# Optimization experiments

Hardware: AMD Instinct MI355X
Metric: run time of the kernel (lower is better)

## Reference

```python
import jax, jax.numpy as jnp
import numpy as np

X_SIZE, Y_SIZE, C_SIZE, H = 4, 2, 3, 128
B, C_CTX, T = 4, 512, 512


def _xavier(key, shape):
    fan_in, fan_out = shape[0], shape[1]
    a = jnp.sqrt(6.0 / (fan_in + fan_out))
    return jax.random.uniform(key, shape, jnp.float32, -a, a)


def setup_inputs() -> dict:
    key = jax.random.key(0)
    ks = jax.random.split(key, 9)
    return {
        "context_x": jax.random.normal(ks[0], (B, C_CTX, X_SIZE), jnp.float32),
        "context_y": jax.random.normal(ks[1], (B, C_CTX, Y_SIZE), jnp.float32),
        "target_x": jax.random.normal(ks[2], (B, T, X_SIZE), jnp.float32),
        "W_in": _xavier(ks[3], (C_SIZE + Y_SIZE, H)),
        "b_in": jnp.zeros((H,), jnp.float32),
        "W_ctx": _xavier(ks[4], (C_SIZE, H)),
        "b_ctx": jnp.zeros((H,), jnp.float32),
        "W_tgt": _xavier(ks[5], (H, H)),
        "b_tgt": jnp.zeros((H,), jnp.float32),
    }


def reference(context_x, context_y, target_x, W_in, b_in, W_ctx, b_ctx, W_tgt, b_tgt):
    ctx_c = context_x[..., :C_SIZE]                         # [B, C, c]
    # value: projected concat of context coords + context values
    enc_in = jnp.concatenate([ctx_c, context_y], axis=-1)   # [B, C, c+y]
    value = enc_in @ W_in + b_in                            # [B, C, H]
    key_ = ctx_c @ W_ctx + b_ctx                            # [B, C, H]
    query = target_x[..., :C_SIZE] @ W_ctx + b_ctx          # [B, T, H]
    # L1-distance attention scores: -sum_h |0.5*(key - query)|
    diff = (key_[:, None, :, :] - query[:, :, None, :]) * 0.5  # [B, T, C, H]
    scores = -jnp.sum(jnp.abs(diff), axis=-1)               # [B, T, C]
    w = jax.nn.softmax(scores, axis=-1)                     # [B, T, C]
    rep = jnp.einsum('btc,bch->bth', w, value)              # [B, T, H]
    return rep @ W_tgt + b_tgt
```

## Files before the change

kernel.cpp:

```cpp
#include <hip/hip_runtime.h>

#define BB 4
#define CC 512
#define TDIM 512
#define HH 128
#define TT 4
#define NW 4
#define CPW 128
#define SC 32
#define NSC 4

__global__ __launch_bounds__(128) void prep_kernel(
    const float* __restrict__ ctx_x, const float* __restrict__ ctx_y,
    const float* __restrict__ tgt_x,
    const float* __restrict__ W_in, const float* __restrict__ b_in,
    const float* __restrict__ W_ctx, const float* __restrict__ b_ctx,
    float* __restrict__ key, float* __restrict__ query, float* __restrict__ value)
{
    int row = blockIdx.x;
    int h   = threadIdx.x;

    float4 cx = ((const float4*)ctx_x)[row];
    float2 cy = ((const float2*)ctx_y)[row];
    float4 tx = ((const float4*)tgt_x)[row];

    float wi0 = W_in[0*HH+h], wi1 = W_in[1*HH+h], wi2 = W_in[2*HH+h];
    float wi3 = W_in[3*HH+h], wi4 = W_in[4*HH+h];
    float wc0 = W_ctx[0*HH+h], wc1 = W_ctx[1*HH+h], wc2 = W_ctx[2*HH+h];
    float bi  = b_in[h], bc = b_ctx[h];

    value[row*HH+h] = fmaf(cx.x,wi0, fmaf(cx.y,wi1, fmaf(cx.z,wi2, fmaf(cy.x,wi3, fmaf(cy.y,wi4, bi)))));
    key  [row*HH+h] = fmaf(cx.x,wc0, fmaf(cx.y,wc1, fmaf(cx.z,wc2, bc)));
    query[row*HH+h] = fmaf(tx.x,wc0, fmaf(tx.y,wc1, fmaf(tx.z,wc2, bc)));
}

__global__ __launch_bounds__(256) void fused_kernel(
    const float* __restrict__ key, const float* __restrict__ query,
    const float* __restrict__ value, const float* __restrict__ W_tgt,
    const float* __restrict__ b_tgt, float* __restrict__ out)
{
    const int bx   = blockIdx.x;
    const int b    = bx >> 7;
    const int t0   = (bx & 127) * TT;
    const int tid  = threadIdx.x;
    const int wv   = tid >> 6;
    const int lane = tid & 63;

    __shared__ __align__(16) float s_w[NW][TT][SC];
    __shared__ __align__(16) float pT_w[NW][SC][TT];
    __shared__ __align__(16) float f_w[NW][TT];
    __shared__ __align__(16) float2 ml_w[NW][TT];
    __shared__ __align__(16) float partial[NW][TT][HH];
    __shared__ __align__(16) float rep[TT][HH];

    const int cl = lane >> 3;
    const int hq = lane & 7;
    float4 qr[TT][4];
    #pragma unroll
    for (int t = 0; t < TT; ++t)
        #pragma unroll
        for (int j = 0; j < 4; ++j)
            qr[t][j] = *(const float4*)&query[(b*TDIM + t0 + t)*HH + j*32 + hq*4];

    const int tg = lane >> 4;
    const int ci = lane & 15;
    const int cs = lane >> 5;
    const int hv = lane & 31;

    float4 acc[TT];
    #pragma unroll
    for (int t = 0; t < TT; ++t) acc[t] = make_float4(0.f,0.f,0.f,0.f);
    float m_run = -1e30f, l_run = 0.f;

    #pragma unroll 1
    for (int scix = 0; scix < NSC; ++scix) {
        const int cbase = wv*CPW + scix*SC;

        {
            const float* kp = &key[(b*CC + cbase + cl*4)*HH];
            float a0[TT], a1[TT], a2[TT], a3[TT];
            #pragma unroll
            for (int t = 0; t < TT; ++t) { a0[t]=0.f; a1[t]=0.f; a2[t]=0.f; a3[t]=0.f; }
            #pragma unroll
            for (int j = 0; j < 4; ++j) {
                const int hb = j*32 + hq*4;
                float4 k0 = *(const float4*)(kp + 0*HH + hb);
                float4 k1 = *(const float4*)(kp + 1*HH + hb);
                float4 k2 = *(const float4*)(kp + 2*HH + hb);
                float4 k3 = *(const float4*)(kp + 3*HH + hb);
                #pragma unroll
                for (int t = 0; t < TT; ++t) {
                    float4 qv = qr[t][j];
                    a0[t] += fabsf(k0.x-qv.x)+fabsf(k0.y-qv.y)+fabsf(k0.z-qv.z)+fabsf(k0.w-qv.w);
                    a1[t] += fabsf(k1.x-qv.x)+fabsf(k1.y-qv.y)+fabsf(k1.z-qv.z)+fabsf(k1.w-qv.w);
                    a2[t] += fabsf(k2.x-qv.x)+fabsf(k2.y-qv.y)+fabsf(k2.z-qv.z)+fabsf(k2.w-qv.w);
                    a3[t] += fabsf(k3.x-qv.x)+fabsf(k3.y-qv.y)+fabsf(k3.z-qv.z)+fabsf(k3.w-qv.w);
                }
            }
            #pragma unroll
            for (int t = 0; t < TT; ++t) {
                float v0=a0[t], v1=a1[t], v2=a2[t], v3=a3[t];
                v0 += __shfl_xor(v0,1); v0 += __shfl_xor(v0,2); v0 += __shfl_xor(v0,4);
                v1 += __shfl_xor(v1,1); v1 += __shfl_xor(v1,2); v1 += __shfl_xor(v1,4);
                v2 += __shfl_xor(v2,1); v2 += __shfl_xor(v2,2); v2 += __shfl_xor(v2,4);
                v3 += __shfl_xor(v3,1); v3 += __shfl_xor(v3,2); v3 += __shfl_xor(v3,4);
                if (hq == 0)
                    *(float4*)&s_w[wv][t][cl*4] =
                        make_float4(-0.5f*v0, -0.5f*v1, -0.5f*v2, -0.5f*v3);
            }
        }

        {
            float x0 = s_w[wv][tg][ci*2], x1 = s_w[wv][tg][ci*2+1];
            float mc = fmaxf(x0, x1);
            mc = fmaxf(mc, __shfl_xor(mc,1)); mc = fmaxf(mc, __shfl_xor(mc,2));
            mc = fmaxf(mc, __shfl_xor(mc,4)); mc = fmaxf(mc, __shfl_xor(mc,8));
            float m_new = fmaxf(m_run, mc);
            float e0 = __expf(x0 - m_new), e1 = __expf(x1 - m_new);
            float sm = e0 + e1;
            sm += __shfl_xor(sm,1); sm += __shfl_xor(sm,2);
            sm += __shfl_xor(sm,4); sm += __shfl_xor(sm,8);
            float f = __expf(m_run - m_new);
            l_run = fmaf(l_run, f, sm);
            m_run = m_new;
            pT_w[wv][ci*2  ][tg] = e0;
            pT_w[wv][ci*2+1][tg] = e1;
            if (ci == 0) f_w[wv][tg] = f;
        }

        {
            const float4 fv = *(const float4*)&f_w[wv][0];
            acc[0].x*=fv.x; acc[0].y*=fv.x; acc[0].z*=fv.x; acc[0].w*=fv.x;
            acc[1].x*=fv.y; acc[1].y*=fv.y; acc[1].z*=fv.y; acc[1].w*=fv.y;
            acc[2].x*=fv.z; acc[2].y*=fv.z; acc[2].z*=fv.z; acc[2].w*=fv.z;
            acc[3].x*=fv.w; acc[3].y*=fv.w; acc[3].z*=fv.w; acc[3].w*=fv.w;
            const float* vp = &value[(b*CC + cbase + cs*16)*HH + hv*4];
            #pragma unroll 4
            for (int i = 0; i < 16; ++i) {
                float4 p4 = *(const float4*)&pT_w[wv][cs*16 + i][0];
                float4 vv = *(const float4*)(vp + i*HH);
                acc[0].x=fmaf(p4.x,vv.x,acc[0].x); acc[0].y=fmaf(p4.x,vv.y,acc[0].y);
                acc[0].z=fmaf(p4.x,vv.z,acc[0].z); acc[0].w=fmaf(p4.x,vv.w,acc[0].w);
                acc[1].x=fmaf(p4.y,vv.x,acc[1].x); acc[1].y=fmaf(p4.y,vv.y,acc[1].y);
                acc[1].z=fmaf(p4.y,vv.z,acc[1].z); acc[1].w=fmaf(p4.y,vv.w,acc[1].w);
                acc[2].x=fmaf(p4.z,vv.x,acc[2].x); acc[2].y=fmaf(p4.z,vv.y,acc[2].y);
                acc[2].z=fmaf(p4.z,vv.z,acc[2].z); acc[2].w=fmaf(p4.z,vv.w,acc[2].w);
                acc[3].x=fmaf(p4.w,vv.x,acc[3].x); acc[3].y=fmaf(p4.w,vv.y,acc[3].y);
                acc[3].z=fmaf(p4.w,vv.z,acc[3].z); acc[3].w=fmaf(p4.w,vv.w,acc[3].w);
            }
        }
    }

    #pragma unroll
    for (int t = 0; t < TT; ++t) {
        acc[t].x += __shfl_xor(acc[t].x, 32);
        acc[t].y += __shfl_xor(acc[t].y, 32);
        acc[t].z += __shfl_xor(acc[t].z, 32);
        acc[t].w += __shfl_xor(acc[t].w, 32);
    }
    if (cs == 0) {
        #pragma unroll
        for (int t = 0; t < TT; ++t)
            *(float4*)&partial[wv][t][hv*4] = acc[t];
    }
    if (ci == 0) ml_w[wv][tg] = make_float2(m_run, l_run);
    __syncthreads();

    for (int e = tid; e < TT*HH; e += 256) {
        const int t = e >> 7, h = e & 127;
        float mw0 = ml_w[0][t].x, lw0 = ml_w[0][t].y;
        float mw1 = ml_w[1][t].x, lw1 = ml_w[1][t].y;
        float mw2 = ml_w[2][t].x, lw2 = ml_w[2][t].y;
        float mw3 = ml_w[3][t].x, lw3 = ml_w[3][t].y;
        float M = fmaxf(fmaxf(mw0, mw1), fmaxf(mw2, mw3));
        float a0 = __expf(mw0-M), a1 = __expf(mw1-M);
        float a2 = __expf(mw2-M), a3 = __expf(mw3-M);
        float L = fmaf(a0,lw0, fmaf(a1,lw1, fmaf(a2,lw2, a3*lw3)));
        float r = a0*partial[0][t][h] + a1*partial[1][t][h]
                + a2*partial[2][t][h] + a3*partial[3][t][h];
        rep[t][h] = r / L;
    }
    __syncthreads();

    {
        const int lt = tid >> 7, h = tid & 127;
        float o0 = b_tgt[h], o1 = o0;
        for (int k = 0; k < HH; k += 4) {
            float4 r0 = *(const float4*)&rep[lt    ][k];
            float4 r1 = *(const float4*)&rep[lt + 2][k];
            float w0 = W_tgt[(k+0)*HH + h];
            float w1 = W_tgt[(k+1)*HH + h];
            float w2 = W_tgt[(k+2)*HH + h];
            float w3 = W_tgt[(k+3)*HH + h];
            o0 = fmaf(r0.x,w0, fmaf(r0.y,w1, fmaf(r0.z,w2, fmaf(r0.w,w3, o0))));
            o1 = fmaf(r1.x,w0, fmaf(r1.y,w1, fmaf(r1.z,w2, fmaf(r1.w,w3, o1))));
        }
        out[(b*TDIM + t0 + lt    )*HH + h] = o0;
        out[(b*TDIM + t0 + lt + 2)*HH + h] = o1;
    }
}

extern "C" void kernel_launch(void* const* d_in, const int* in_sizes, int n_in,
                              void* d_out, int out_size, void* d_ws, size_t ws_size,
                              hipStream_t stream) {
    const float* ctx_x = (const float*)d_in[0];
    const float* ctx_y = (const float*)d_in[1];
    const float* tgt_x = (const float*)d_in[2];
    const float* W_in  = (const float*)d_in[3];
    const float* b_in  = (const float*)d_in[4];
    const float* W_ctx = (const float*)d_in[5];
    const float* b_ctx = (const float*)d_in[6];
    const float* W_tgt = (const float*)d_in[7];
    const float* b_tgt = (const float*)d_in[8];

    float* ws    = (float*)d_ws;
    float* key   = ws;
    float* query = ws + 1*BB*CC*HH;
    float* value = ws + 2*BB*CC*HH;

    prep_kernel<<<BB*CC, 128, 0, stream>>>(ctx_x, ctx_y, tgt_x,
                                           W_in, b_in, W_ctx, b_ctx,
                                           key, query, value);
    fused_kernel<<<BB*(TDIM/TT), 256, 0, stream>>>(key, query, value,
                                                   W_tgt, b_tgt, (float*)d_out);
}
```

Before: 36.37 us.

## Double targets per block and replace online softmax with full-row two-phase softmax

Each block now handles 8 targets with 512 threads: two groups of four waves, each group covering 4 targets over the full context split four ways. Each wave computes all 128 scores for its slice first, then does a single softmax and value accumulation, so the running max/rescale steps of the online softmax go away. Score and probability buffers are reused as rep and partial storage to hold shared-memory size down. The block count halves to 256, which may leave part of the GPU idle. Larger per-wave score buffers also add LDS traffic and register pressure.

```diff
diff --git a/kernel.cpp b/kernel.cpp
--- a/kernel.cpp
+++ b/kernel.cpp
@@ -4,11 +4,9 @@
 #define CC 512
 #define TDIM 512
 #define HH 128
-#define TT 4
-#define NW 4
+#define TT 8
+#define NR 4
 #define CPW 128
-#define SC 32
-#define NSC 4
 
 __global__ __launch_bounds__(128) void prep_kernel(
     const float* __restrict__ ctx_x, const float* __restrict__ ctx_y,
@@ -34,150 +32,138 @@
     query[row*HH+h] = fmaf(tx.x,wc0, fmaf(tx.y,wc1, fmaf(tx.z,wc2, bc)));
 }
 
-__global__ __launch_bounds__(256) void fused_kernel(
+__global__ __launch_bounds__(512) void fused_kernel(
     const float* __restrict__ key, const float* __restrict__ query,
     const float* __restrict__ value, const float* __restrict__ W_tgt,
     const float* __restrict__ b_tgt, float* __restrict__ out)
 {
     const int bx   = blockIdx.x;
-    const int b    = bx >> 7;
-    const int t0   = (bx & 127) * TT;
+    const int b    = bx >> 6;
+    const int t0   = (bx & 63) * TT;
     const int tid  = threadIdx.x;
-    const int wv   = tid >> 6;
+    const int wave = tid >> 6;
+    const int cr   = wave & 3;
+    const int th   = wave >> 2;
     const int lane = tid & 63;
 
-    __shared__ __align__(16) float s_w[NW][TT][SC];
-    __shared__ __align__(16) float pT_w[NW][SC][TT];
-    __shared__ __align__(16) float f_w[NW][TT];
-    __shared__ __align__(16) float2 ml_w[NW][TT];
-    __shared__ __align__(16) float partial[NW][TT][HH];
-    __shared__ __align__(16) float rep[TT][HH];
+    __shared__ __align__(16) float sbuf[8][4][128];
+    __shared__ __align__(16) float pTbuf[8][128][4];
+    __shared__ __align__(16) float2 ml[8][4];
+
+    float (*rep)[HH]        = (float (*)[HH])&sbuf[0][0][0];
+    float (*partial)[4][HH] = (float (*)[4][HH])&pTbuf[0][0][0];
 
     const int cl = lane >> 3;
     const int hq = lane & 7;
-    float4 qr[TT][4];
+    float4 qr[4][4];
     #pragma unroll
-    for (int t = 0; t < TT; ++t)
+    for (int tt = 0; tt < 4; ++tt)
         #pragma unroll
         for (int j = 0; j < 4; ++j)
-            qr[t][j] = *(const float4*)&query[(b*TDIM + t0 + t)*HH + j*32 + hq*4];
-
-    const int tg = lane >> 4;
-    const int ci = lane & 15;
-    const int cs = lane >> 5;
-    const int hv = lane & 31;
-
-    float4 acc[TT];
+            qr[tt][j] = *(const float4*)&query[(b*TDIM + t0 + th*4 + tt)*HH + j*32 + hq*4];
+
+    #pragma unroll 1
+    for (int pp = 0; pp < 4; ++pp) {
+        const int crow = cr*CPW + pp*32 + cl*4;
+        const float* kp = &key[(b*CC + crow)*HH];
+        float a0[4], a1[4], a2[4], a3[4];
+        #pragma unroll
+        for (int tt = 0; tt < 4; ++tt) { a0[tt]=0.f; a1[tt]=0.f; a2[tt]=0.f; a3[tt]=0.f; }
+        #pragma unroll
+        for (int j = 0; j < 4; ++j) {
+            const int hb = j*32 + hq*4;
+            float4 k0 = *(const float4*)(kp + 0*HH + hb);
+            float4 k1 = *(const float4*)(kp + 1*HH + hb);
+            float4 k2 = *(const float4*)(kp + 2*HH + hb);
+            float4 k3 = *(const float4*)(kp + 3*HH + hb);
+            #pragma unroll
+            for (int tt = 0; tt < 4; ++tt) {
+                float4 qv = qr[tt][j];
+                a0[tt] += fabsf(k0.x-qv.x)+fabsf(k0.y-qv.y)+fabsf(k0.z-qv.z)+fabsf(k0.w-qv.w);
+                a1[tt] += fabsf(k1.x-qv.x)+fabsf(k1.y-qv.y)+fabsf(k1.z-qv.z)+fabsf(k1.w-qv.w);
+                a2[tt] += fabsf(k2.x-qv.x)+fabsf(k2.y-qv.y)+fabsf(k2.z-qv.z)+fabsf(k2.w-qv.w);
+                a3[tt] += fabsf(k3.x-qv.x)+fabsf(k3.y-qv.y)+fabsf(k3.z-qv.z)+fabsf(k3.w-qv.w);
+            }
+        }
+        #pragma unroll
+        for (int tt = 0; tt < 4; ++tt) {
+            float v0=a0[tt], v1=a1[tt], v2=a2[tt], v3=a3[tt];
+            v0 += __shfl_xor(v0,1); v0 += __shfl_xor(v0,2); v0 += __shfl_xor(v0,4);
+            v1 += __shfl_xor(v1,1); v1 += __shfl_xor(v1,2); v1 += __shfl_xor(v1,4);
+            v2 += __shfl_xor(v2,1); v2 += __shfl_xor(v2,2); v2 += __shfl_xor(v2,4);
+            v3 += __shfl_xor(v3,1); v3 += __shfl_xor(v3,2); v3 += __shfl_xor(v3,4);
+            if (hq == 0)
+                *(float4*)&sbuf[wave][tt][pp*32 + cl*4] =
+                    make_float4(-0.5f*v0, -0.5f*v1, -0.5f*v2, -0.5f*v3);
+        }
+    }
+
+    {
+        const int tg = lane >> 4, ci = lane & 15;
+        float4 x0 = *(const float4*)&sbuf[wave][tg][ci*8];
+        float4 x1 = *(const float4*)&sbuf[wave][tg][ci*8 + 4];
+        float m = fmaxf(fmaxf(fmaxf(x0.x,x0.y), fmaxf(x0.z,x0.w)),
+                        fmaxf(fmaxf(x1.x,x1.y), fmaxf(x1.z,x1.w)));
+        m = fmaxf(m, __shfl_xor(m,1)); m = fmaxf(m, __shfl_xor(m,2));
+        m = fmaxf(m, __shfl_xor(m,4)); m = fmaxf(m, __shfl_xor(m,8));
+        float e0 = __expf(x0.x-m), e1 = __expf(x0.y-m), e2 = __expf(x0.z-m), e3 = __expf(x0.w-m);
+        float e4 = __expf(x1.x-m), e5 = __expf(x1.y-m), e6 = __expf(x1.z-m), e7 = __expf(x1.w-m);
+        float sm = ((e0+e1)+(e2+e3)) + ((e4+e5)+(e6+e7));
+        sm += __shfl_xor(sm,1); sm += __shfl_xor(sm,2);
+        sm += __shfl_xor(sm,4); sm += __shfl_xor(sm,8);
+        pTbuf[wave][ci*8+0][tg] = e0;  pTbuf[wave][ci*8+1][tg] = e1;
+        pTbuf[wave][ci*8+2][tg] = e2;  pTbuf[wave][ci*8+3][tg] = e3;
+        pTbuf[wave][ci*8+4][tg] = e4;  pTbuf[wave][ci*8+5][tg] = e5;
+        pTbuf[wave][ci*8+6][tg] = e6;  pTbuf[wave][ci*8+7][tg] = e7;
+        if (ci == 0) ml[wave][tg] = make_float2(m, sm);
+    }
+
+    const int cs = lane >> 5, hv = lane & 31;
+    {
+        float4 acc[4];
+        #pragma unroll
+        for (int tt = 0; tt < 4; ++tt) acc[tt] = make_float4(0.f,0.f,0.f,0.f);
+        const float* vp = &value[(b*CC + cr*CPW + cs*64)*HH + hv*4];
+        #pragma unroll 4
+        for (int i = 0; i < 64; ++i) {
+            float4 p4 = *(const float4*)&pTbuf[wave][cs*64 + i][0];
+            float4 vv = *(const float4*)(vp + i*HH);
+            acc[0].x=fmaf(p4.x,vv.x,acc[0].x); acc[0].y=fmaf(p4.x,vv.y,acc[0].y);
+            acc[0].z=fmaf(p4.x,vv.z,acc[0].z); acc[0].w=fmaf(p4.x,vv.w,acc[0].w);
+            acc[1].x=fmaf(p4.y,vv.x,acc[1].x); acc[1].y=fmaf(p4.y,vv.y,acc[1].y);
+            acc[1].z=fmaf(p4.y,vv.z,acc[1].z); acc[1].w=fmaf(p4.y,vv.w,acc[1].w);
+            acc[2].x=fmaf(p4.z,vv.x,acc[2].x); acc[2].y=fmaf(p4.z,vv.y,acc[2].y);
+            acc[2].z=fmaf(p4.z,vv.z,acc[2].z); acc[2].w=fmaf(p4.z,vv.w,acc[2].w);
+            acc[3].x=fmaf(p4.w,vv.x,acc[3].x); acc[3].y=fmaf(p4.w,vv.y,acc[3].y);
+            acc[3].z=fmaf(p4.w,vv.z,acc[3].z); acc[3].w=fmaf(p4.w,vv.w,acc[3].w);
+        }
+        #pragma unroll
+        for (int tt = 0; tt < 4; ++tt) {
+            acc[tt].x += __shfl_xor(acc[tt].x, 32);
+            acc[tt].y += __shfl_xor(acc[tt].y, 32);
+            acc[tt].z += __shfl_xor(acc[tt].z, 32);
+            acc[tt].w += __shfl_xor(acc[tt].w, 32);
+        }
+        if (cs == 0) {
+            #pragma unroll
+            for (int tt = 0; tt < 4; ++tt)
+                *(float4*)&partial[wave][tt][hv*4] = acc[tt];
+        }
+    }
+    __syncthreads();
+
     #pragma unroll
-    for (int t = 0; t < TT; ++t) acc[t] = make_float4(0.f,0.f,0.f,0.f);
-    float m_run = -1e30f, l_run = 0.f;
-
-    #pragma unroll 1
-    for (int scix = 0; scix < NSC; ++scix) {
-        const int cbase = wv*CPW + scix*SC;
-
-        {
-            const float* kp = &key[(b*CC + cbase + cl*4)*HH];
-            float a0[TT], a1[TT], a2[TT], a3[TT];
-            #pragma unroll
-            for (int t = 0; t < TT; ++t) { a0[t]=0.f; a1[t]=0.f; a2[t]=0.f; a3[t]=0.f; }
-            #pragma unroll
-            for (int j = 0; j < 4; ++j) {
-                const int hb = j*32 + hq*4;
-                float4 k0 = *(const float4*)(kp + 0*HH + hb);
-                float4 k1 = *(const float4*)(kp + 1*HH + hb);
-                float4 k2 = *(const float4*)(kp + 2*HH + hb);
-                float4 k3 = *(const float4*)(kp + 3*HH + hb);
-                #pragma unroll
-                for (int t = 0; t < TT; ++t) {
-                    float4 qv = qr[t][j];
-                    a0[t] += fabsf(k0.x-qv.x)+fabsf(k0.y-qv.y)+fabsf(k0.z-qv.z)+fabsf(k0.w-qv.w);
-                    a1[t] += fabsf(k1.x-qv.x)+fabsf(k1.y-qv.y)+fabsf(k1.z-qv.z)+fabsf(k1.w-qv.w);
-                    a2[t] += fabsf(k2.x-qv.x)+fabsf(k2.y-qv.y)+fabsf(k2.z-qv.z)+fabsf(k2.w-qv.w);
-                    a3[t] += fabsf(k3.x-qv.x)+fabsf(k3.y-qv.y)+fabsf(k3.z-qv.z)+fabsf(k3.w-qv.w);
-                }
-            }
-            #pragma unroll
-            for (int t = 0; t < TT; ++t) {
-                float v0=a0[t], v1=a1[t], v2=a2[t], v3=a3[t];
-                v0 += __shfl_xor(v0,1); v0 += __shfl_xor(v0,2); v0 += __shfl_xor(v0,4);
-                v1 += __shfl_xor(v1,1); v1 += __shfl_xor(v1,2); v1 += __shfl_xor(v1,4);
-                v2 += __shfl_xor(v2,1); v2 += __shfl_xor(v2,2); v2 += __shfl_xor(v2,4);
-                v3 += __shfl_xor(v3,1); v3 += __shfl_xor(v3,2); v3 += __shfl_xor(v3,4);
-                if (hq == 0)
-                    *(float4*)&s_w[wv][t][cl*4] =
-                        make_float4(-0.5f*v0, -0.5f*v1, -0.5f*v2, -0.5f*v3);
-            }
-        }
-
-        {
-            float x0 = s_w[wv][tg][ci*2], x1 = s_w[wv][tg][ci*2+1];
-            float mc = fmaxf(x0, x1);
-            mc = fmaxf(mc, __shfl_xor(mc,1)); mc = fmaxf(mc, __shfl_xor(mc,2));
-            mc = fmaxf(mc, __shfl_xor(mc,4)); mc = fmaxf(mc, __shfl_xor(mc,8));
-            float m_new = fmaxf(m_run, mc);
-            float e0 = __expf(x0 - m_new), e1 = __expf(x1 - m_new);
-            float sm = e0 + e1;
-            sm += __shfl_xor(sm,1); sm += __shfl_xor(sm,2);
-            sm += __shfl_xor(sm,4); sm += __shfl_xor(sm,8);
-            float f = __expf(m_run - m_new);
-            l_run = fmaf(l_run, f, sm);
-            m_run = m_new;
-            pT_w[wv][ci*2  ][tg] = e0;
-            pT_w[wv][ci*2+1][tg] = e1;
-            if (ci == 0) f_w[wv][tg] = f;
-        }
-
-        {
-            const float4 fv = *(const float4*)&f_w[wv][0];
-            acc[0].x*=fv.x; acc[0].y*=fv.x; acc[0].z*=fv.x; acc[0].w*=fv.x;
-            acc[1].x*=fv.y; acc[1].y*=fv.y; acc[1].z*=fv.y; acc[1].w*=fv.y;
-            acc[2].x*=fv.z; acc[2].y*=fv.z; acc[2].z*=fv.z; acc[2].w*=fv.z;
-            acc[3].x*=fv.w; acc[3].y*=fv.w; acc[3].z*=fv.w; acc[3].w*=fv.w;
-            const float* vp = &value[(b*CC + cbase + cs*16)*HH + hv*4];
-            #pragma unroll 4
-            for (int i = 0; i < 16; ++i) {
-                float4 p4 = *(const float4*)&pT_w[wv][cs*16 + i][0];
-                float4 vv = *(const float4*)(vp + i*HH);
-                acc[0].x=fmaf(p4.x,vv.x,acc[0].x); acc[0].y=fmaf(p4.x,vv.y,acc[0].y);
-                acc[0].z=fmaf(p4.x,vv.z,acc[0].z); acc[0].w=fmaf(p4.x,vv.w,acc[0].w);
-                acc[1].x=fmaf(p4.y,vv.x,acc[1].x); acc[1].y=fmaf(p4.y,vv.y,acc[1].y);
-                acc[1].z=fmaf(p4.y,vv.z,acc[1].z); acc[1].w=fmaf(p4.y,vv.w,acc[1].w);
-                acc[2].x=fmaf(p4.z,vv.x,acc[2].x); acc[2].y=fmaf(p4.z,vv.y,acc[2].y);
-                acc[2].z=fmaf(p4.z,vv.z,acc[2].z); acc[2].w=fmaf(p4.z,vv.w,acc[2].w);
-                acc[3].x=fmaf(p4.w,vv.x,acc[3].x); acc[3].y=fmaf(p4.w,vv.y,acc[3].y);
-                acc[3].z=fmaf(p4.w,vv.z,acc[3].z); acc[3].w=fmaf(p4.w,vv.w,acc[3].w);
-            }
-        }
-    }
-
-    #pragma unroll
-    for (int t = 0; t < TT; ++t) {
-        acc[t].x += __shfl_xor(acc[t].x, 32);
-        acc[t].y += __shfl_xor(acc[t].y, 32);
-        acc[t].z += __shfl_xor(acc[t].z, 32);
-        acc[t].w += __shfl_xor(acc[t].w, 32);
-    }
-    if (cs == 0) {
-        #pragma unroll
-        for (int t = 0; t < TT; ++t)
-            *(float4*)&partial[wv][t][hv*4] = acc[t];
-    }
-    if (ci == 0) ml_w[wv][tg] = make_float2(m_run, l_run);
-    __syncthreads();
-
-    for (int e = tid; e < TT*HH; e += 256) {
+    for (int e = tid; e < TT*HH; e += 512) {
         const int t = e >> 7, h = e & 127;
-        float mw0 = ml_w[0][t].x, lw0 = ml_w[0][t].y;
-        float mw1 = ml_w[1][t].x, lw1 = ml_w[1][t].y;
-        float mw2 = ml_w[2][t].x, lw2 = ml_w[2][t].y;
-        float mw3 = ml_w[3][t].x, lw3 = ml_w[3][t].y;
-        float M = fmaxf(fmaxf(mw0, mw1), fmaxf(mw2, mw3));
-        float a0 = __expf(mw0-M), a1 = __expf(mw1-M);
-        float a2 = __expf(mw2-M), a3 = __expf(mw3-M);
-        float L = fmaf(a0,lw0, fmaf(a1,lw1, fmaf(a2,lw2, a3*lw3)));
-        float r = a0*partial[0][t][h] + a1*partial[1][t][h]
-                + a2*partial[2][t][h] + a3*partial[3][t][h];
+        const int thh = t >> 2, tt = t & 3;
+        float2 q0 = ml[thh*4+0][tt], q1 = ml[thh*4+1][tt];
+        float2 q2 = ml[thh*4+2][tt], q3 = ml[thh*4+3][tt];
+        float M = fmaxf(fmaxf(q0.x,q1.x), fmaxf(q2.x,q3.x));
+        float a0 = __expf(q0.x-M), a1 = __expf(q1.x-M);
+        float a2 = __expf(q2.x-M), a3 = __expf(q3.x-M);
+        float L = fmaf(a0,q0.y, fmaf(a1,q1.y, fmaf(a2,q2.y, a3*q3.y)));
+        float r = a0*partial[thh*4+0][tt][h] + a1*partial[thh*4+1][tt][h]
+                + a2*partial[thh*4+2][tt][h] + a3*partial[thh*4+3][tt][h];
         rep[t][h] = r / L;
     }
     __syncthreads();
@@ -187,7 +173,7 @@
         float o0 = b_tgt[h], o1 = o0;
         for (int k = 0; k < HH; k += 4) {
             float4 r0 = *(const float4*)&rep[lt    ][k];
-            float4 r1 = *(const float4*)&rep[lt + 2][k];
+            float4 r1 = *(const float4*)&rep[lt + 4][k];
             float w0 = W_tgt[(k+0)*HH + h];
             float w1 = W_tgt[(k+1)*HH + h];
             float w2 = W_tgt[(k+2)*HH + h];
@@ -196,7 +182,7 @@
             o1 = fmaf(r1.x,w0, fmaf(r1.y,w1, fmaf(r1.z,w2, fmaf(r1.w,w3, o1))));
         }
         out[(b*TDIM + t0 + lt    )*HH + h] = o0;
-        out[(b*TDIM + t0 + lt + 2)*HH + h] = o1;
+        out[(b*TDIM + t0 + lt + 4)*HH + h] = o1;
     }
 }
 
@@ -221,6 +207,6 @@
     prep_kernel<<<BB*CC, 128, 0, stream>>>(ctx_x, ctx_y, tgt_x,
                                            W_in, b_in, W_ctx, b_ctx,
                                            key, query, value);
-    fused_kernel<<<BB*(TDIM/TT), 256, 0, stream>>>(key, query, value,
+    fused_kernel<<<BB*(TDIM/TT), 512, 0, stream>>>(key, query, value,
                                                    W_tgt, b_tgt, (float*)d_out);
 }
```

Measured after the change: 32.49 us. 1.12x faster.
